# Optimization experiments

Measured on AMD Instinct MI355X. Metric: run time of the kernel, lower is better.

Reference implementation:

```python
import jax, jax.numpy as jnp
import numpy as np


def bilinear_sampler(img, flow):
    """Warp img (B,H,W,C) by per-pixel flow (B,H,W,2): sample at (x+u, y+v).
    Border handling: indices clipped to the image (edge padding)."""
    B, H, W, C = img.shape
    gy, gx = jnp.meshgrid(jnp.arange(H, dtype=img.dtype),
                          jnp.arange(W, dtype=img.dtype), indexing='ij')
    x = gx[None] + flow[..., 0]  # (B,H,W)
    y = gy[None] + flow[..., 1]
    x0f = jnp.floor(x)
    y0f = jnp.floor(y)
    wx = x - x0f  # fractional parts, differentiable w.r.t. flow
    wy = y - y0f
    x0 = jnp.clip(x0f.astype(jnp.int32), 0, W - 1)
    x1 = jnp.clip(x0f.astype(jnp.int32) + 1, 0, W - 1)
    y0 = jnp.clip(y0f.astype(jnp.int32), 0, H - 1)
    y1 = jnp.clip(y0f.astype(jnp.int32) + 1, 0, H - 1)
    b = jnp.arange(B)[:, None, None]
    Ia = img[b, y0, x0]  # (B,H,W,C)
    Ib = img[b, y1, x0]
    Ic = img[b, y0, x1]
    Id = img[b, y1, x1]
    wx = wx[..., None]
    wy = wy[..., None]
    return (Ia * (1 - wx) * (1 - wy) + Ib * (1 - wx) * wy
            + Ic * wx * (1 - wy) + Id * wx * wy)


def setup_inputs() -> dict:
    key = jax.random.key(0)
    k1, k2, k3, k4, k5, k6 = jax.random.split(key, 6)
    B, H, W = 8, 512, 512
    return {
        't': jax.random.uniform(k1, (B, 1, 1, 1), dtype=jnp.float32),
        'I0': jax.random.uniform(k2, (B, H, W, 3), dtype=jnp.float32),
        'I1': jax.random.uniform(k3, (B, H, W, 3), dtype=jnp.float32),
        'interp': jax.random.normal(k4, (B, H, W, 5), dtype=jnp.float32),
        'Fhat_t0': jax.random.normal(k5, (B, H, W, 2), dtype=jnp.float32),
        'Fhat_t1': jax.random.normal(k6, (B, H, W, 2), dtype=jnp.float32),
    }


def reference(t, I0, I1, interp, Fhat_t0, Fhat_t1):
    Ft0 = interp[..., 0:2] + Fhat_t0
    Ft1 = interp[..., 2:4] + Fhat_t1
    Vt0 = jax.nn.sigmoid(interp[..., 4:5])  # (B,H,W,1) -> broadcasts over RGB
    Vt1 = 1.0 - Vt0
    g0 = bilinear_sampler(I0, Ft0)
    g1 = bilinear_sampler(I1, Ft1)
    eps = 1e-12
    w0 = (1.0 - t) * Vt0
    w1 = t * Vt1
    It = (w0 * g0 + w1 * g1) / (w0 + w1 + eps)
    return It
```

## Files before the change

### kernel.cpp

```cpp
#include <hip/hip_runtime.h>

constexpr int B_ = 8;
constexpr int H_ = 512;
constexpr int W_ = 512;
constexpr int HW_ = H_ * W_;
constexpr int NPIX = B_ * HW_;

__device__ __forceinline__ void bilin3(const float* __restrict__ img,
                                       float xx, float yy,
                                       float& r, float& g, float& b) {
    float x0f = floorf(xx);
    float y0f = floorf(yy);
    float wx = xx - x0f;
    float wy = yy - y0f;
    int x0 = min(max((int)x0f, 0), W_ - 1);
    int x1 = min(max((int)x0f + 1, 0), W_ - 1);
    int y0 = min(max((int)y0f, 0), H_ - 1);
    int y1 = min(max((int)y0f + 1, 0), H_ - 1);

    const float* pa = img + ((size_t)y0 * W_ + x0) * 3;
    const float* pb = img + ((size_t)y1 * W_ + x0) * 3;
    const float* pc = img + ((size_t)y0 * W_ + x1) * 3;
    const float* pd = img + ((size_t)y1 * W_ + x1) * 3;

    float wa = (1.0f - wx) * (1.0f - wy);
    float wb = (1.0f - wx) * wy;
    float wc = wx * (1.0f - wy);
    float wd = wx * wy;

    r = pa[0] * wa + pb[0] * wb + pc[0] * wc + pd[0] * wd;
    g = pa[1] * wa + pb[1] * wb + pc[1] * wc + pd[1] * wd;
    b = pa[2] * wa + pb[2] * wb + pc[2] * wc + pd[2] * wd;
}

__global__ __launch_bounds__(256) void frame_interp_kernel(
    const float* __restrict__ t,
    const float* __restrict__ I0,
    const float* __restrict__ I1,
    const float* __restrict__ interp,
    const float* __restrict__ F0,
    const float* __restrict__ F1,
    float* __restrict__ out)
{
    int idx = blockIdx.x * blockDim.x + threadIdx.x;
    if (idx >= NPIX) return;

    int b  = idx >> 18;
    int p  = idx & (HW_ - 1);
    int y  = p >> 9;
    int x  = p & (W_ - 1);

    const float* ip = interp + (size_t)idx * 5;
    float it0 = ip[0], it1 = ip[1], it2 = ip[2], it3 = ip[3], it4 = ip[4];

    const float2* f0p = (const float2*)(F0 + (size_t)idx * 2);
    const float2* f1p = (const float2*)(F1 + (size_t)idx * 2);
    float2 f0 = *f0p;
    float2 f1 = *f1p;

    float tb = t[b];

    float ft0x = it0 + f0.x;
    float ft0y = it1 + f0.y;
    float ft1x = it2 + f1.x;
    float ft1y = it3 + f1.y;

    float vt0 = 1.0f / (1.0f + expf(-it4));
    float vt1 = 1.0f - vt0;

    const float* img0 = I0 + (size_t)b * HW_ * 3;
    const float* img1 = I1 + (size_t)b * HW_ * 3;

    float g0r, g0g, g0b, g1r, g1g, g1b;
    bilin3(img0, (float)x + ft0x, (float)y + ft0y, g0r, g0g, g0b);
    bilin3(img1, (float)x + ft1x, (float)y + ft1y, g1r, g1g, g1b);

    float w0 = (1.0f - tb) * vt0;
    float w1 = tb * vt1;
    float inv = 1.0f / (w0 + w1 + 1e-12f);

    float* op = out + (size_t)idx * 3;
    op[0] = (w0 * g0r + w1 * g1r) * inv;
    op[1] = (w0 * g0g + w1 * g1g) * inv;
    op[2] = (w0 * g0b + w1 * g1b) * inv;
}

extern "C" void kernel_launch(void* const* d_in, const int* in_sizes, int n_in,
                              void* d_out, int out_size, void* d_ws, size_t ws_size,
                              hipStream_t stream) {
    const float* t      = (const float*)d_in[0];
    const float* I0     = (const float*)d_in[1];
    const float* I1     = (const float*)d_in[2];
    const float* interp = (const float*)d_in[3];
    const float* F0     = (const float*)d_in[4];
    const float* F1     = (const float*)d_in[5];
    float* out = (float*)d_out;

    int threads = 256;
    int blocks = (NPIX + threads - 1) / threads;
    frame_interp_kernel<<<blocks, threads, 0, stream>>>(t, I0, I1, interp, F0, F1, out);
}
```

Before: 183.7 us.

## Process four pixels per thread with vectorized nontemporal loads and paired texel fetches

```diff
diff --git a/kernel.cpp b/kernel.cpp
--- a/kernel.cpp
+++ b/kernel.cpp
@@ -5,32 +5,46 @@
 constexpr int W_ = 512;
 constexpr int HW_ = H_ * W_;
 constexpr int NPIX = B_ * HW_;
+constexpr int PPT = 4;
+constexpr int NTHREADS_TOTAL = NPIX / PPT;
 
-__device__ __forceinline__ void bilin3(const float* __restrict__ img,
-                                       float xx, float yy,
-                                       float& r, float& g, float& b) {
+typedef float f4 __attribute__((ext_vector_type(4)));
+
+__device__ __forceinline__ void sample3(const float* __restrict__ img,
+                                        float xx, float yy,
+                                        float g[3]) {
     float x0f = floorf(xx);
     float y0f = floorf(yy);
     float wx = xx - x0f;
     float wy = yy - y0f;
-    int x0 = min(max((int)x0f, 0), W_ - 1);
-    int x1 = min(max((int)x0f + 1, 0), W_ - 1);
-    int y0 = min(max((int)y0f, 0), H_ - 1);
-    int y1 = min(max((int)y0f + 1, 0), H_ - 1);
+    int ix = (int)x0f;
+    int iy = (int)y0f;
+    int x0 = min(max(ix, 0), W_ - 1);
+    int x1 = min(max(ix + 1, 0), W_ - 1);
+    int xb = min(max(ix, 0), W_ - 2);
+    int y0 = min(max(iy, 0), H_ - 1);
+    int y1 = min(max(iy + 1, 0), H_ - 1);
 
-    const float* pa = img + ((size_t)y0 * W_ + x0) * 3;
-    const float* pb = img + ((size_t)y1 * W_ + x0) * 3;
-    const float* pc = img + ((size_t)y0 * W_ + x1) * 3;
-    const float* pd = img + ((size_t)y1 * W_ + x1) * 3;
+    float a[6], c[6];
+    __builtin_memcpy(a, img + ((size_t)y0 * W_ + xb) * 3, 24);
+    __builtin_memcpy(c, img + ((size_t)y1 * W_ + xb) * 3, 24);
 
-    float wa = (1.0f - wx) * (1.0f - wy);
-    float wb = (1.0f - wx) * wy;
-    float wc = wx * (1.0f - wy);
-    float wd = wx * wy;
+    bool hi0 = (x0 != xb);
+    bool hi1 = (x1 != xb);
 
-    r = pa[0] * wa + pb[0] * wb + pc[0] * wc + pd[0] * wd;
-    g = pa[1] * wa + pb[1] * wb + pc[1] * wc + pd[1] * wd;
-    b = pa[2] * wa + pb[2] * wb + pc[2] * wc + pd[2] * wd;
+    float w00 = (1.0f - wx) * (1.0f - wy);
+    float w01 = wx * (1.0f - wy);
+    float w10 = (1.0f - wx) * wy;
+    float w11 = wx * wy;
+
+    #pragma unroll
+    for (int ch = 0; ch < 3; ++ch) {
+        float p00 = hi0 ? a[3 + ch] : a[ch];
+        float p01 = hi1 ? a[3 + ch] : a[ch];
+        float p10 = hi0 ? c[3 + ch] : c[ch];
+        float p11 = hi1 ? c[3 + ch] : c[ch];
+        g[ch] = p00 * w00 + p01 * w01 + p10 * w10 + p11 * w11;
+    }
 }
 
 __global__ __launch_bounds__(256) void frame_interp_kernel(
@@ -42,47 +56,68 @@
     const float* __restrict__ F1,
     float* __restrict__ out)
 {
-    int idx = blockIdx.x * blockDim.x + threadIdx.x;
-    if (idx >= NPIX) return;
-
-    int b  = idx >> 18;
-    int p  = idx & (HW_ - 1);
-    int y  = p >> 9;
-    int x  = p & (W_ - 1);
-
-    const float* ip = interp + (size_t)idx * 5;
-    float it0 = ip[0], it1 = ip[1], it2 = ip[2], it3 = ip[3], it4 = ip[4];
-
-    const float2* f0p = (const float2*)(F0 + (size_t)idx * 2);
-    const float2* f1p = (const float2*)(F1 + (size_t)idx * 2);
-    float2 f0 = *f0p;
-    float2 f1 = *f1p;
+    int tid = blockIdx.x * blockDim.x + threadIdx.x;
+    if (tid >= NTHREADS_TOTAL) return;
+    int p4 = tid * PPT;
+    int b    = p4 >> 18;
+    int prow = (p4 & (HW_ - 1)) >> 9;
+    int pcol = p4 & (W_ - 1);
 
     float tb = t[b];
 
-    float ft0x = it0 + f0.x;
-    float ft0y = it1 + f0.y;
-    float ft1x = it2 + f1.x;
-    float ft1y = it3 + f1.y;
-
-    float vt0 = 1.0f / (1.0f + expf(-it4));
-    float vt1 = 1.0f - vt0;
+    float ibuf[20];
+    {
+        const f4* s = (const f4*)(interp + (size_t)p4 * 5);
+        f4* d = (f4*)ibuf;
+        #pragma unroll
+        for (int k = 0; k < 5; ++k) d[k] = __builtin_nontemporal_load(s + k);
+    }
+    float fb0[8], fb1[8];
+    {
+        const f4* s0 = (const f4*)(F0 + (size_t)p4 * 2);
+        const f4* s1 = (const f4*)(F1 + (size_t)p4 * 2);
+        f4* d0 = (f4*)fb0;
+        f4* d1 = (f4*)fb1;
+        #pragma unroll
+        for (int k = 0; k < 2; ++k) {
+            d0[k] = __builtin_nontemporal_load(s0 + k);
+            d1[k] = __builtin_nontemporal_load(s1 + k);
+        }
+    }
 
     const float* img0 = I0 + (size_t)b * HW_ * 3;
     const float* img1 = I1 + (size_t)b * HW_ * 3;
 
-    float g0r, g0g, g0b, g1r, g1g, g1b;
-    bilin3(img0, (float)x + ft0x, (float)y + ft0y, g0r, g0g, g0b);
-    bilin3(img1, (float)x + ft1x, (float)y + ft1y, g1r, g1g, g1b);
+    float obuf[12];
 
-    float w0 = (1.0f - tb) * vt0;
-    float w1 = tb * vt1;
-    float inv = 1.0f / (w0 + w1 + 1e-12f);
+    #pragma unroll
+    for (int j = 0; j < PPT; ++j) {
+        float ft0x = ibuf[j * 5 + 0] + fb0[j * 2 + 0];
+        float ft0y = ibuf[j * 5 + 1] + fb0[j * 2 + 1];
+        float ft1x = ibuf[j * 5 + 2] + fb1[j * 2 + 0];
+        float ft1y = ibuf[j * 5 + 3] + fb1[j * 2 + 1];
+        float vt0  = 1.0f / (1.0f + expf(-ibuf[j * 5 + 4]));
 
-    float* op = out + (size_t)idx * 3;
-    op[0] = (w0 * g0r + w1 * g1r) * inv;
-    op[1] = (w0 * g0g + w1 * g1g) * inv;
-    op[2] = (w0 * g0b + w1 * g1b) * inv;
+        float xP = (float)(pcol + j);
+        float yP = (float)prow;
+
+        float g0[3], g1[3];
+        sample3(img0, xP + ft0x, yP + ft0y, g0);
+        sample3(img1, xP + ft1x, yP + ft1y, g1);
+
+        float w0 = (1.0f - tb) * vt0;
+        float w1 = tb * (1.0f - vt0);
+        float inv = 1.0f / (w0 + w1 + 1e-12f);
+
+        obuf[j * 3 + 0] = (w0 * g0[0] + w1 * g1[0]) * inv;
+        obuf[j * 3 + 1] = (w0 * g0[1] + w1 * g1[1]) * inv;
+        obuf[j * 3 + 2] = (w0 * g0[2] + w1 * g1[2]) * inv;
+    }
+
+    f4* o = (f4*)(out + (size_t)p4 * 3);
+    const f4* ob = (const f4*)obuf;
+    #pragma unroll
+    for (int k = 0; k < 3; ++k) __builtin_nontemporal_store(ob[k], o + k);
 }
 
 extern "C" void kernel_launch(void* const* d_in, const int* in_sizes, int n_in,
@@ -97,6 +132,6 @@
     float* out = (float*)d_out;
 
     int threads = 256;
-    int blocks = (NPIX + threads - 1) / threads;
+    int blocks = NTHREADS_TOTAL / threads;
     frame_interp_kernel<<<blocks, threads, 0, stream>>>(t, I0, I1, interp, F0, F1, out);
 }
```

Result: slower. 221.2 us (+20.5%).
